# Performance work log

Measured on AMD Instinct MI355X. Metric: run time of the kernel, lower is better.

Reference implementation:

```python
import jax, jax.numpy as jnp
import numpy as np

B = 16384          # batch
N_IN = 1024        # input nodes
L = 8              # layers
W_LAYER = 512      # nodes per layer (fan-in and fan-out)
N_NODES = N_IN + L * W_LAYER  # 5120 total nodes in shared buffer
MASK_DENSITY = 0.25


def setup_inputs() -> dict:
    key = jax.random.key(0)
    kx, kw, km, kb = jax.random.split(key, 4)
    x = jax.random.normal(kx, (B, N_IN), dtype=jnp.float32)
    W = jax.random.normal(kw, (L, W_LAYER, W_LAYER), dtype=jnp.float32) * 0.05
    mask = (jax.random.uniform(km, (L, W_LAYER, W_LAYER)) < MASK_DENSITY).astype(jnp.float32)
    bias = jax.random.normal(kb, (L, W_LAYER), dtype=jnp.float32) * 0.01
    rng = np.random.default_rng(0)
    # layer l gathers from nodes already computed: indices in [0, N_IN + l*W_LAYER)
    in_idx = np.stack([rng.integers(0, N_IN + l * W_LAYER, size=W_LAYER) for l in range(L)]).astype(np.int32)
    # layer l writes its own contiguous node slots
    out_idx = np.stack([np.arange(N_IN + l * W_LAYER, N_IN + (l + 1) * W_LAYER) for l in range(L)]).astype(np.int32)
    return {"x": x, "W": W, "mask": mask, "bias": bias,
            "in_idx": jnp.asarray(in_idx), "out_idx": jnp.asarray(out_idx)}


def reference(x, W, mask, bias, in_idx, out_idx):
    # shared node-value buffer, inputs written into first N_IN columns
    values = jnp.zeros((x.shape[0], N_NODES), dtype=x.dtype)
    values = values.at[:, :N_IN].set(x)

    def step(vals, layer):
        idx_in, idx_out, Wl, ml, bl = layer
        node_inputs = vals[:, idx_in]                       # [B, W_LAYER] gather
        h = jax.nn.relu(node_inputs @ (Wl * ml).T + bl)     # masked linear + ReLU
        return vals.at[:, idx_out].set(h), None             # scatter back

    values, _ = jax.lax.scan(step, values, (in_idx, out_idx, W, mask, bias))
    return values[:, out_idx[-1]]  # output nodes = last layer's nodes
```

## Files before the change

kernel.cpp:

```cpp
#include <hip/hip_runtime.h>
#include <stdint.h>

typedef unsigned short u16;
typedef unsigned int   u32;
typedef short s16x8 __attribute__((ext_vector_type(8)));
typedef float f32x4 __attribute__((ext_vector_type(4)));

#define NB    16384
#define NIN   1024
#define WLY   512
#define NLAY  8
#define NNODE (NIN + NLAY * WLY)
#define BN    64

__device__ __forceinline__ u16 f2bf(float f) {
  union { float f; u32 u; } c; c.f = f;
  return (u16)((c.u + 0x7fffu + ((c.u >> 16) & 1u)) >> 16);
}

__global__ void prep_w(const float* __restrict__ W, const float* __restrict__ Mk,
                       u16* __restrict__ Wm) {
  int id   = blockIdx.x * 256 + threadIdx.x;
  int lane = id & 63;
  int chunk = id >> 6;
  int kf = chunk & 1;
  int mb = (chunk >> 1) & 31;
  int kt = (chunk >> 6) & 7;
  int l  = chunk >> 9;
  int m  = (mb << 4) + (lane & 15);
  int k0 = (kt << 6) + (kf << 5) + ((lane >> 4) << 3);
  size_t base = ((size_t)l << 18) + (size_t)m * 512 + k0;
  const float4* w4 = (const float4*)(W + base);
  const float4* k4 = (const float4*)(Mk + base);
  float4 w0 = w4[0], w1 = w4[1];
  float4 k0v = k4[0], k1v = k4[1];
  u32 p0 = (u32)f2bf(w0.x * k0v.x) | ((u32)f2bf(w0.y * k0v.y) << 16);
  u32 p1 = (u32)f2bf(w0.z * k0v.z) | ((u32)f2bf(w0.w * k0v.w) << 16);
  u32 p2 = (u32)f2bf(w1.x * k1v.x) | ((u32)f2bf(w1.y * k1v.y) << 16);
  u32 p3 = (u32)f2bf(w1.z * k1v.z) | ((u32)f2bf(w1.w * k1v.w) << 16);
  uint4 v; v.x = p0; v.y = p1; v.z = p2; v.w = p3;
  *(uint4*)(Wm + ((size_t)chunk << 9) + (lane << 3)) = v;
}

__global__ __launch_bounds__(512, 2) void fused_net(
    const float* __restrict__ x, const u16* __restrict__ Wfrag,
    const float* __restrict__ bias, const int* __restrict__ in_idx,
    u16* __restrict__ V, float* __restrict__ out) {

  __shared__ __align__(16) u16 Graw[2][4096];
  __shared__ __align__(16) u16 Gswz[2][4096];
  __shared__ int   idx_s[512];
  __shared__ float bias_s[512];
  __shared__ __align__(16) u16 Ebuf[512 * 72];

  int t = threadIdx.x;
  int lane = t & 63, w = t >> 6;
  int mlane = lane & 15, g = lane >> 4;
  int n0 = blockIdx.x * BN;

  float* xt = (float*)Ebuf;
  for (int cc = 0; cc < 8; ++cc) {
    #pragma unroll
    for (int it = 0; it < 4; ++it) {
      int cl = t + it * 512;
      int b = cl >> 5, p = cl & 31;
      *(float4*)(xt + b * 128 + (p << 2)) =
          *(const float4*)(x + (size_t)(n0 + b) * 1024 + cc * 128 + (p << 2));
    }
    __syncthreads();
    {
      int c = t >> 2, seg = t & 3;
      u32 p[8];
      #pragma unroll
      for (int i = 0; i < 8; ++i) {
        u16 lo = f2bf(xt[(seg * 16 + 2 * i) * 128 + c]);
        u16 hi = f2bf(xt[(seg * 16 + 2 * i + 1) * 128 + c]);
        p[i] = (u32)lo | ((u32)hi << 16);
      }
      u16* dst = V + (size_t)(cc * 128 + c) * NB + n0 + seg * 16;
      uint4 v0; v0.x = p[0]; v0.y = p[1]; v0.z = p[2]; v0.w = p[3];
      uint4 v1; v1.x = p[4]; v1.y = p[5]; v1.z = p[6]; v1.w = p[7];
      *(uint4*)dst = v0;
      *(uint4*)(dst + 8) = v1;
    }
    __syncthreads();
  }

#define STAGE(KT, BUF) do {                                                    \
    int k_ = (w << 3) + (lane >> 3);                                           \
    int row_ = idx_s[((KT) << 6) + k_];                                        \
    const u16* src_ = V + (size_t)row_ * NB + n0 + ((lane & 7) << 3);          \
    __builtin_amdgcn_global_load_lds(                                          \
        (const __attribute__((address_space(1))) u32*)src_,                    \
        (__attribute__((address_space(3))) u32*)(&Graw[BUF][w << 9]), 16, 0, 0); \
  } while (0)

  for (int l = 0; l < NLAY; ++l) {
    idx_s[t]  = in_idx[(l << 9) + t];
    bias_s[t] = bias[(l << 9) + t];
    __syncthreads();

    const u16* Wl = Wfrag + ((size_t)l << 18);
    int node_out = NIN + l * WLY;

    f32x4 acc[4][4];
    #pragma unroll
    for (int i = 0; i < 4; ++i)
      #pragma unroll
      for (int j = 0; j < 4; ++j)
        acc[i][j] = (f32x4){0.f, 0.f, 0.f, 0.f};

    STAGE(0, 0);
    __syncthreads();

    #pragma unroll
    for (int kt = 0; kt < 8; ++kt) {
      const int cur = kt & 1;
      s16x8 a[4][2];
      #pragma unroll
      for (int mb = 0; mb < 4; ++mb)
        #pragma unroll
        for (int kf = 0; kf < 2; ++kf)
          a[mb][kf] = *(const s16x8*)(Wl +
              ((size_t)(((kt * 32 + (w << 2) + mb) << 1) + kf) << 9) + (lane << 3));
      {
        int n = t & 63, kc = t >> 6;
        u32 p[4];
        #pragma unroll
        for (int i = 0; i < 4; ++i) {
          u16 lo = Graw[cur][(kc * 8 + 2 * i) * 64 + n];
          u16 hi = Graw[cur][(kc * 8 + 2 * i + 1) * 64 + n];
          p[i] = (u32)lo | ((u32)hi << 16);
        }
        uint4 vv; vv.x = p[0]; vv.y = p[1]; vv.z = p[2]; vv.w = p[3];
        *(uint4*)((char*)Gswz[cur] + n * 128 + ((kc * 16) ^ ((n & 7) << 4))) = vv;
      }
      if (kt < 7) { STAGE(kt + 1, cur ^ 1); }
      __syncthreads();
      #pragma unroll
      for (int kf = 0; kf < 2; ++kf) {
        s16x8 bfr[4];
        #pragma unroll
        for (int nf = 0; nf < 4; ++nf) {
          int n = (nf << 4) + mlane;
          bfr[nf] = *(const s16x8*)((const char*)Gswz[cur] + n * 128 +
                                    (((kf << 6) + (g << 4)) ^ ((n & 7) << 4)));
        }
        #pragma unroll
        for (int mb = 0; mb < 4; ++mb)
          #pragma unroll
          for (int nf = 0; nf < 4; ++nf)
            acc[mb][nf] = __builtin_amdgcn_mfma_f32_16x16x32_bf16(
                a[mb][kf], bfr[nf], acc[mb][nf], 0, 0, 0);
      }
    }

    if (l < NLAY - 1) {
      #pragma unroll
      for (int mb = 0; mb < 4; ++mb)
        #pragma unroll
        for (int nf = 0; nf < 4; ++nf)
          #pragma unroll
          for (int r = 0; r < 4; ++r) {
            int m = (w << 6) + (mb << 4) + (g << 2) + r;
            int n = (nf << 4) + mlane;
            Ebuf[m * 72 + n] = f2bf(fmaxf(acc[mb][nf][r] + bias_s[m], 0.f));
          }
      __syncthreads();
      #pragma unroll
      for (int it = 0; it < 8; ++it) {
        int row = (it << 6) + (t >> 3), part = t & 7;
        *(uint4*)(V + (size_t)(node_out + row) * NB + n0 + (part << 3)) =
            *(uint4*)(&Ebuf[row * 72 + (part << 3)]);
      }
      __syncthreads();
    } else {
      #pragma unroll
      for (int mb = 0; mb < 4; ++mb)
        #pragma unroll
        for (int nf = 0; nf < 4; ++nf) {
          int n = (nf << 4) + mlane;
          int m0f = (w << 6) + (mb << 4) + (g << 2);
          float4 v;
          v.x = fmaxf(acc[mb][nf][0] + bias_s[m0f + 0], 0.f);
          v.y = fmaxf(acc[mb][nf][1] + bias_s[m0f + 1], 0.f);
          v.z = fmaxf(acc[mb][nf][2] + bias_s[m0f + 2], 0.f);
          v.w = fmaxf(acc[mb][nf][3] + bias_s[m0f + 3], 0.f);
          *(float4*)(out + (size_t)(n0 + n) * 512 + m0f) = v;
        }
    }
  }
#undef STAGE
}

extern "C" void kernel_launch(void* const* d_in, const int* in_sizes, int n_in,
                              void* d_out, int out_size, void* d_ws, size_t ws_size,
                              hipStream_t stream) {
  (void)in_sizes; (void)n_in; (void)out_size; (void)ws_size;
  const float* x    = (const float*)d_in[0];
  const float* W    = (const float*)d_in[1];
  const float* Mk   = (const float*)d_in[2];
  const float* bias = (const float*)d_in[3];
  const int*  inidx = (const int*)d_in[4];
  float* out = (float*)d_out;

  char* ws = (char*)d_ws;
  u16* V     = (u16*)ws;
  u16* Wfrag = (u16*)(ws + (size_t)NNODE * NB * 2);

  prep_w<<<dim3(1024), 256, 0, stream>>>(W, Mk, Wfrag);
  fused_net<<<dim3(256), 512, 0, stream>>>(x, Wfrag, bias, inidx, V, out);
}
```

Measured before the change: 124.7 us.

## Deepen gather pipeline to four stages with manual waitcnt scheduling

Replaces the double-buffered gather/GEMM loop with a 4-deep Graw ring buffer, prefetching three k-tiles ahead and double-buffering the weight fragment registers. Explicit vmcnt/lgkmcnt waits and sched barriers replace the __syncthreads calls so global gathers overlap with the transpose and the MFMA work. The epilogue drops its barriers by having each wave write back only its own rows. The last layer is now staged through LDS in bf16 so stores to the output are coalesced. The tradeoffs are more LDS and registers, possible occupancy loss, bf16 rounding of the final output, and fragile hand-counted waits.

```diff
diff --git a/kernel.cpp b/kernel.cpp
--- a/kernel.cpp
+++ b/kernel.cpp
@@ -17,6 +17,16 @@
   union { float f; u32 u; } c; c.f = f;
   return (u16)((c.u + 0x7fffu + ((c.u >> 16) & 1u)) >> 16);
 }
+__device__ __forceinline__ float bf2f(u16 h) {
+  union { u32 u; float f; } c; c.u = ((u32)h) << 16;
+  return c.f;
+}
+
+#define SCHED0() __builtin_amdgcn_sched_barrier(0)
+#define BAR()    __builtin_amdgcn_s_barrier()
+#define WAITVM_IMPL(N) asm volatile("s_waitcnt vmcnt(" #N ")" ::: "memory")
+#define WAITVM(N) WAITVM_IMPL(N)
+#define WAITLG()  asm volatile("s_waitcnt lgkmcnt(0)" ::: "memory")
 
 __global__ void prep_w(const float* __restrict__ W, const float* __restrict__ Mk,
                        u16* __restrict__ Wm) {
@@ -47,11 +57,11 @@
     const float* __restrict__ bias, const int* __restrict__ in_idx,
     u16* __restrict__ V, float* __restrict__ out) {
 
-  __shared__ __align__(16) u16 Graw[2][4096];
+  __shared__ __align__(16) u16 Graw[4][4096];
   __shared__ __align__(16) u16 Gswz[2][4096];
+  __shared__ __align__(16) u16 Ebuf[512 * 72];
   __shared__ int   idx_s[512];
   __shared__ float bias_s[512];
-  __shared__ __align__(16) u16 Ebuf[512 * 72];
 
   int t = threadIdx.x;
   int lane = t & 63, w = t >> 6;
@@ -86,13 +96,63 @@
     __syncthreads();
   }
 
-#define STAGE(KT, BUF) do {                                                    \
+#define STAGE(KT, R) do {                                                      \
     int k_ = (w << 3) + (lane >> 3);                                           \
     int row_ = idx_s[((KT) << 6) + k_];                                        \
     const u16* src_ = V + (size_t)row_ * NB + n0 + ((lane & 7) << 3);          \
     __builtin_amdgcn_global_load_lds(                                          \
         (const __attribute__((address_space(1))) u32*)src_,                    \
-        (__attribute__((address_space(3))) u32*)(&Graw[BUF][w << 9]), 16, 0, 0); \
+        (__attribute__((address_space(3))) u32*)(&Graw[R][w << 9]), 16, 0, 0); \
+  } while (0)
+
+#define LDA(KTN) do {                                                          \
+    _Pragma("unroll") for (int mb = 0; mb < 4; ++mb)                           \
+    _Pragma("unroll") for (int kf = 0; kf < 2; ++kf)                           \
+      a[(KTN) & 1][mb][kf] = *(const s16x8*)(Wl +                              \
+          ((size_t)((((KTN) * 32 + (w << 2) + mb) << 1) + kf) << 9) +          \
+          (lane << 3));                                                        \
+  } while (0)
+
+#define TRANSP(KT) do {                                                        \
+    int n_ = t & 63, kc_ = t >> 6;                                             \
+    const u16* gb_ = Graw[(KT) & 3];                                           \
+    u32 p0_ = (u32)gb_[(kc_ * 8 + 0) * 64 + n_] |                              \
+              ((u32)gb_[(kc_ * 8 + 1) * 64 + n_] << 16);                       \
+    u32 p1_ = (u32)gb_[(kc_ * 8 + 2) * 64 + n_] |                              \
+              ((u32)gb_[(kc_ * 8 + 3) * 64 + n_] << 16);                       \
+    u32 p2_ = (u32)gb_[(kc_ * 8 + 4) * 64 + n_] |                              \
+              ((u32)gb_[(kc_ * 8 + 5) * 64 + n_] << 16);                       \
+    u32 p3_ = (u32)gb_[(kc_ * 8 + 6) * 64 + n_] |                              \
+              ((u32)gb_[(kc_ * 8 + 7) * 64 + n_] << 16);                       \
+    uint4 vv_; vv_.x = p0_; vv_.y = p1_; vv_.z = p2_; vv_.w = p3_;             \
+    *(uint4*)((char*)Gswz[(KT) & 1] + n_ * 128 +                               \
+              ((kc_ * 16) ^ ((n_ & 7) << 4))) = vv_;                           \
+  } while (0)
+
+#define MM(KT) do {                                                            \
+    const char* gs_ = (const char*)Gswz[(KT) & 1];                             \
+    _Pragma("unroll") for (int kf = 0; kf < 2; ++kf) {                         \
+      s16x8 bfr[4];                                                            \
+      _Pragma("unroll") for (int nf = 0; nf < 4; ++nf) {                       \
+        int n_ = (nf << 4) + mlane;                                            \
+        bfr[nf] = *(const s16x8*)(gs_ + n_ * 128 +                             \
+                  (((kf << 6) + (g << 4)) ^ ((n_ & 7) << 4)));                 \
+      }                                                                        \
+      _Pragma("unroll") for (int mb = 0; mb < 4; ++mb)                         \
+      _Pragma("unroll") for (int nf = 0; nf < 4; ++nf)                         \
+        acc[mb][nf] = __builtin_amdgcn_mfma_f32_16x16x32_bf16(                 \
+            a[(KT) & 1][mb][kf], bfr[nf], acc[mb][nf], 0, 0, 0);               \
+    }                                                                          \
+  } while (0)
+
+#define BODY(KT, VMN, PRE, POST) do {                                          \
+    if (PRE) { LDA((KT) + 1); }                                                \
+    SCHED0(); WAITVM(VMN); SCHED0();                                           \
+    BAR();                                                                     \
+    if (POST) { STAGE((KT) + 3, ((KT) + 3) & 3); }                             \
+    TRANSP(KT);                                                                \
+    SCHED0(); WAITLG(); BAR(); SCHED0();                                       \
+    MM(KT);                                                                    \
   } while (0)
 
   for (int l = 0; l < NLAY; ++l) {
@@ -110,50 +170,21 @@
       for (int j = 0; j < 4; ++j)
         acc[i][j] = (f32x4){0.f, 0.f, 0.f, 0.f};
 
-    STAGE(0, 0);
-    __syncthreads();
-
-    #pragma unroll
-    for (int kt = 0; kt < 8; ++kt) {
-      const int cur = kt & 1;
-      s16x8 a[4][2];
-      #pragma unroll
-      for (int mb = 0; mb < 4; ++mb)
-        #pragma unroll
-        for (int kf = 0; kf < 2; ++kf)
-          a[mb][kf] = *(const s16x8*)(Wl +
-              ((size_t)(((kt * 32 + (w << 2) + mb) << 1) + kf) << 9) + (lane << 3));
-      {
-        int n = t & 63, kc = t >> 6;
-        u32 p[4];
-        #pragma unroll
-        for (int i = 0; i < 4; ++i) {
-          u16 lo = Graw[cur][(kc * 8 + 2 * i) * 64 + n];
-          u16 hi = Graw[cur][(kc * 8 + 2 * i + 1) * 64 + n];
-          p[i] = (u32)lo | ((u32)hi << 16);
-        }
-        uint4 vv; vv.x = p[0]; vv.y = p[1]; vv.z = p[2]; vv.w = p[3];
-        *(uint4*)((char*)Gswz[cur] + n * 128 + ((kc * 16) ^ ((n & 7) << 4))) = vv;
-      }
-      if (kt < 7) { STAGE(kt + 1, cur ^ 1); }
-      __syncthreads();
-      #pragma unroll
-      for (int kf = 0; kf < 2; ++kf) {
-        s16x8 bfr[4];
-        #pragma unroll
-        for (int nf = 0; nf < 4; ++nf) {
-          int n = (nf << 4) + mlane;
-          bfr[nf] = *(const s16x8*)((const char*)Gswz[cur] + n * 128 +
-                                    (((kf << 6) + (g << 4)) ^ ((n & 7) << 4)));
-        }
-        #pragma unroll
-        for (int mb = 0; mb < 4; ++mb)
-          #pragma unroll
-          for (int nf = 0; nf < 4; ++nf)
-            acc[mb][nf] = __builtin_amdgcn_mfma_f32_16x16x32_bf16(
-                a[mb][kf], bfr[nf], acc[mb][nf], 0, 0, 0);
-      }
-    }
+    s16x8 a[2][4][2];
+
+    STAGE(0, 0); STAGE(1, 1); STAGE(2, 2);
+    SCHED0();
+    LDA(0);
+    SCHED0();
+
+    BODY(0, 8, 1, 1);
+    BODY(1, 9, 1, 1);
+    BODY(2, 9, 1, 1);
+    BODY(3, 9, 1, 1);
+    BODY(4, 9, 1, 1);
+    BODY(5, 9, 1, 0);
+    BODY(6, 8, 1, 0);
+    BODY(7, 0, 0, 0);
 
     if (l < NLAY - 1) {
       #pragma unroll
@@ -166,31 +197,44 @@
             int n = (nf << 4) + mlane;
             Ebuf[m * 72 + n] = f2bf(fmaxf(acc[mb][nf][r] + bias_s[m], 0.f));
           }
-      __syncthreads();
       #pragma unroll
       for (int it = 0; it < 8; ++it) {
-        int row = (it << 6) + (t >> 3), part = t & 7;
-        *(uint4*)(V + (size_t)(node_out + row) * NB + n0 + (part << 3)) =
-            *(uint4*)(&Ebuf[row * 72 + (part << 3)]);
+        int row = (w << 6) + (it << 3) + (lane >> 3);
+        uint4 vv = *(uint4*)(Ebuf + row * 72 + ((lane & 7) << 3));
+        *(uint4*)(V + (size_t)(node_out + row) * NB + n0 + ((lane & 7) << 3)) = vv;
       }
-      __syncthreads();
     } else {
       #pragma unroll
       for (int mb = 0; mb < 4; ++mb)
         #pragma unroll
-        for (int nf = 0; nf < 4; ++nf) {
-          int n = (nf << 4) + mlane;
-          int m0f = (w << 6) + (mb << 4) + (g << 2);
+        for (int nf = 0; nf < 4; ++nf)
+          #pragma unroll
+          for (int r = 0; r < 4; ++r) {
+            int m = (w << 6) + (mb << 4) + (g << 2) + r;
+            int n = (nf << 4) + mlane;
+            Ebuf[m * 66 + n] = f2bf(fmaxf(acc[mb][nf][r] + bias_s[m], 0.f));
+          }
+      __syncthreads();
+      #pragma unroll
+      for (int pn = 0; pn < 8; ++pn)
+        #pragma unroll
+        for (int h = 0; h < 2; ++h) {
+          int n = (t >> 6) + (pn << 3);
+          int mbase = ((t & 63) << 2) + (h << 8);
           float4 v;
-          v.x = fmaxf(acc[mb][nf][0] + bias_s[m0f + 0], 0.f);
-          v.y = fmaxf(acc[mb][nf][1] + bias_s[m0f + 1], 0.f);
-          v.z = fmaxf(acc[mb][nf][2] + bias_s[m0f + 2], 0.f);
-          v.w = fmaxf(acc[mb][nf][3] + bias_s[m0f + 3], 0.f);
-          *(float4*)(out + (size_t)(n0 + n) * 512 + m0f) = v;
+          v.x = bf2f(Ebuf[(mbase + 0) * 66 + n]);
+          v.y = bf2f(Ebuf[(mbase + 1) * 66 + n]);
+          v.z = bf2f(Ebuf[(mbase + 2) * 66 + n]);
+          v.w = bf2f(Ebuf[(mbase + 3) * 66 + n]);
+          *(float4*)(out + (size_t)(n0 + n) * 512 + mbase) = v;
         }
     }
   }
 #undef STAGE
+#undef LDA
+#undef TRANSP
+#undef MM
+#undef BODY
 }
 
 extern "C" void kernel_launch(void* const* d_in, const int* in_sizes, int n_in,
```

After: 123.2 us. No clear change (-1.2%).

## Halve batch tile to 32, shrink LDS pool, raise occupancy

Applied to the files above, without the earlier changes.

Batch tile per block drops from 64 to 32 columns, doubling the grid to 512 blocks and asking for 4 blocks per CU. LDS shrinks to a single 16 KB pool. The epilogue LDS staging buffer is removed, so activations go straight to global memory as strided 2-byte stores. Bias and index arrays are read from global into registers rather than shared memory. The aim is more resident waves and lower LDS and barrier cost, but each block now does fewer MFMAs per weight fragment loaded, doubling total weight traffic, and the direct scattered 2-byte writes are poorly coalesced.

```diff
diff --git a/kernel.cpp b/kernel.cpp
--- a/kernel.cpp
+++ b/kernel.cpp
@@ -11,7 +11,7 @@
 #define WLY   512
 #define NLAY  8
 #define NNODE (NIN + NLAY * WLY)
-#define BN    64
+#define BN    32
 
 __device__ __forceinline__ u16 f2bf(float f) {
   union { float f; u32 u; } c; c.f = f;
@@ -42,26 +42,24 @@
   *(uint4*)(Wm + ((size_t)chunk << 9) + (lane << 3)) = v;
 }
 
-__global__ __launch_bounds__(512, 2) void fused_net(
+__global__ __launch_bounds__(512, 4) void fused_net(
     const float* __restrict__ x, const u16* __restrict__ Wfrag,
     const float* __restrict__ bias, const int* __restrict__ in_idx,
     u16* __restrict__ V, float* __restrict__ out) {
 
-  __shared__ __align__(16) u16 Graw[2][4096];
-  __shared__ __align__(16) u16 Gswz[2][4096];
-  __shared__ int   idx_s[512];
-  __shared__ float bias_s[512];
-  __shared__ __align__(16) u16 Ebuf[512 * 72];
+  __shared__ __align__(16) u16 pool[8192];
+  u16* Graw0 = pool;
+  u16* Gswz0 = pool + 4096;
 
   int t = threadIdx.x;
   int lane = t & 63, w = t >> 6;
   int mlane = lane & 15, g = lane >> 4;
   int n0 = blockIdx.x * BN;
 
-  float* xt = (float*)Ebuf;
+  float* xt = (float*)pool;
   for (int cc = 0; cc < 8; ++cc) {
     #pragma unroll
-    for (int it = 0; it < 4; ++it) {
+    for (int it = 0; it < 2; ++it) {
       int cl = t + it * 512;
       int b = cl >> 5, p = cl & 31;
       *(float4*)(xt + b * 128 + (p << 2)) =
@@ -70,127 +68,132 @@
     __syncthreads();
     {
       int c = t >> 2, seg = t & 3;
-      u32 p[8];
-      #pragma unroll
-      for (int i = 0; i < 8; ++i) {
-        u16 lo = f2bf(xt[(seg * 16 + 2 * i) * 128 + c]);
-        u16 hi = f2bf(xt[(seg * 16 + 2 * i + 1) * 128 + c]);
-        p[i] = (u32)lo | ((u32)hi << 16);
-      }
-      u16* dst = V + (size_t)(cc * 128 + c) * NB + n0 + seg * 16;
-      uint4 v0; v0.x = p[0]; v0.y = p[1]; v0.z = p[2]; v0.w = p[3];
-      uint4 v1; v1.x = p[4]; v1.y = p[5]; v1.z = p[6]; v1.w = p[7];
-      *(uint4*)dst = v0;
-      *(uint4*)(dst + 8) = v1;
+      u32 pk[4];
+      #pragma unroll
+      for (int i = 0; i < 4; ++i) {
+        u16 lo = f2bf(xt[(seg * 8 + 2 * i) * 128 + c]);
+        u16 hi = f2bf(xt[(seg * 8 + 2 * i + 1) * 128 + c]);
+        pk[i] = (u32)lo | ((u32)hi << 16);
+      }
+      uint4 vv; vv.x = pk[0]; vv.y = pk[1]; vv.z = pk[2]; vv.w = pk[3];
+      *(uint4*)(V + (size_t)(cc * 128 + c) * NB + n0 + (seg << 3)) = vv;
     }
     __syncthreads();
   }
 
-#define STAGE(KT, BUF) do {                                                    \
-    int k_ = (w << 3) + (lane >> 3);                                           \
-    int row_ = idx_s[((KT) << 6) + k_];                                        \
-    const u16* src_ = V + (size_t)row_ * NB + n0 + ((lane & 7) << 3);          \
-    __builtin_amdgcn_global_load_lds(                                          \
-        (const __attribute__((address_space(1))) u32*)src_,                    \
-        (__attribute__((address_space(3))) u32*)(&Graw[BUF][w << 9]), 16, 0, 0); \
-  } while (0)
-
   for (int l = 0; l < NLAY; ++l) {
-    idx_s[t]  = in_idx[(l << 9) + t];
-    bias_s[t] = bias[(l << 9) + t];
-    __syncthreads();
-
+    __syncthreads();
+
+    int rowv[8];
+    if (w < 4) {
+      #pragma unroll
+      for (int kt = 0; kt < 8; ++kt)
+        rowv[kt] = in_idx[(l << 9) + (kt << 6) + (w << 4) + (lane >> 2)];
+    }
     const u16* Wl = Wfrag + ((size_t)l << 18);
     int node_out = NIN + l * WLY;
 
-    f32x4 acc[4][4];
+    f32x4 acc[4][2];
     #pragma unroll
     for (int i = 0; i < 4; ++i)
       #pragma unroll
-      for (int j = 0; j < 4; ++j)
+      for (int j = 0; j < 2; ++j)
         acc[i][j] = (f32x4){0.f, 0.f, 0.f, 0.f};
+
+    s16x8 a[4][2];
+
+#define STAGE(KT, BUF) do {                                                    \
+    if (w < 4) {                                                               \
+      const u16* src_ = V + (size_t)rowv[KT] * NB + n0 + ((lane & 3) << 3);    \
+      __builtin_amdgcn_global_load_lds(                                        \
+          (const __attribute__((address_space(1))) u32*)src_,                  \
+          (__attribute__((address_space(3))) u32*)(Graw0 + ((BUF) << 11) +     \
+                                                  (w << 9)), 16, 0, 0);        \
+    }                                                                          \
+  } while (0)
 
     STAGE(0, 0);
     __syncthreads();
 
     #pragma unroll
     for (int kt = 0; kt < 8; ++kt) {
-      const int cur = kt & 1;
-      s16x8 a[4][2];
       #pragma unroll
       for (int mb = 0; mb < 4; ++mb)
         #pragma unroll
         for (int kf = 0; kf < 2; ++kf)
           a[mb][kf] = *(const s16x8*)(Wl +
-              ((size_t)(((kt * 32 + (w << 2) + mb) << 1) + kf) << 9) + (lane << 3));
+              ((size_t)(((kt * 32 + (w << 2) + mb) << 1) + kf) << 9) +
+              (lane << 3));
+      if (kt < 7) STAGE(kt + 1, (kt + 1) & 1);
       {
-        int n = t & 63, kc = t >> 6;
-        u32 p[4];
-        #pragma unroll
-        for (int i = 0; i < 4; ++i) {
-          u16 lo = Graw[cur][(kc * 8 + 2 * i) * 64 + n];
-          u16 hi = Graw[cur][(kc * 8 + 2 * i + 1) * 64 + n];
-          p[i] = (u32)lo | ((u32)hi << 16);
+        const u16* gb = Graw0 + ((kt & 1) << 11);
+        int n_ = t & 31, kc4 = t >> 5;
+        u16 v0 = gb[(kc4 * 4 + 0) * 32 + n_];
+        u16 v1 = gb[(kc4 * 4 + 1) * 32 + n_];
+        u16 v2 = gb[(kc4 * 4 + 2) * 32 + n_];
+        u16 v3 = gb[(kc4 * 4 + 3) * 32 + n_];
+        u32 p0 = (u32)v0 | ((u32)v1 << 16);
+        u32 p1 = (u32)v2 | ((u32)v3 << 16);
+        uint2 pr; pr.x = p0; pr.y = p1;
+        *(uint2*)((char*)(Gswz0 + ((kt & 1) << 11)) + n_ * 128 +
+                  ((kc4 << 3) ^ ((n_ & 7) << 4))) = pr;
+      }
+      __syncthreads();
+      {
+        const char* gs = (const char*)(Gswz0 + ((kt & 1) << 11));
+        #pragma unroll
+        for (int kf = 0; kf < 2; ++kf) {
+          s16x8 bfr[2];
+          #pragma unroll
+          for (int nf = 0; nf < 2; ++nf) {
+            int n_ = (nf << 4) + mlane;
+            bfr[nf] = *(const s16x8*)(gs + n_ * 128 +
+                      (((kf << 6) + (g << 4)) ^ ((n_ & 7) << 4)));
+          }
+          #pragma unroll
+          for (int mb = 0; mb < 4; ++mb)
+            #pragma unroll
+            for (int nf = 0; nf < 2; ++nf)
+              acc[mb][nf] = __builtin_amdgcn_mfma_f32_16x16x32_bf16(
+                  a[mb][kf], bfr[nf], acc[mb][nf], 0, 0, 0);
         }
-        uint4 vv; vv.x = p[0]; vv.y = p[1]; vv.z = p[2]; vv.w = p[3];
-        *(uint4*)((char*)Gswz[cur] + n * 128 + ((kc * 16) ^ ((n & 7) << 4))) = vv;
-      }
-      if (kt < 7) { STAGE(kt + 1, cur ^ 1); }
-      __syncthreads();
-      #pragma unroll
-      for (int kf = 0; kf < 2; ++kf) {
-        s16x8 bfr[4];
-        #pragma unroll
-        for (int nf = 0; nf < 4; ++nf) {
-          int n = (nf << 4) + mlane;
-          bfr[nf] = *(const s16x8*)((const char*)Gswz[cur] + n * 128 +
-                                    (((kf << 6) + (g << 4)) ^ ((n & 7) << 4)));
+      }
+    }
+#undef STAGE
+
+    if (l < NLAY - 1) {
+      #pragma unroll
+      for (int mb = 0; mb < 4; ++mb) {
+        float4 bv = *(const float4*)(bias + (l << 9) + (w << 6) + (mb << 4) + (g << 2));
+        float bvr[4] = {bv.x, bv.y, bv.z, bv.w};
+        #pragma unroll
+        for (int nf = 0; nf < 2; ++nf) {
+          int n_ = (nf << 4) + mlane;
+          u16* vp = V + (size_t)(node_out + (w << 6) + (mb << 4) + (g << 2)) * NB
+                      + n0 + n_;
+          #pragma unroll
+          for (int r = 0; r < 4; ++r)
+            vp[(size_t)r * NB] = f2bf(fmaxf(acc[mb][nf][r] + bvr[r], 0.f));
         }
-        #pragma unroll
-        for (int mb = 0; mb < 4; ++mb)
-          #pragma unroll
-          for (int nf = 0; nf < 4; ++nf)
-            acc[mb][nf] = __builtin_amdgcn_mfma_f32_16x16x32_bf16(
-                a[mb][kf], bfr[nf], acc[mb][nf], 0, 0, 0);
-      }
-    }
-
-    if (l < NLAY - 1) {
-      #pragma unroll
-      for (int mb = 0; mb < 4; ++mb)
-        #pragma unroll
-        for (int nf = 0; nf < 4; ++nf)
-          #pragma unroll
-          for (int r = 0; r < 4; ++r) {
-            int m = (w << 6) + (mb << 4) + (g << 2) + r;
-            int n = (nf << 4) + mlane;
-            Ebuf[m * 72 + n] = f2bf(fmaxf(acc[mb][nf][r] + bias_s[m], 0.f));
-          }
-      __syncthreads();
-      #pragma unroll
-      for (int it = 0; it < 8; ++it) {
-        int row = (it << 6) + (t >> 3), part = t & 7;
-        *(uint4*)(V + (size_t)(node_out + row) * NB + n0 + (part << 3)) =
-            *(uint4*)(&Ebuf[row * 72 + (part << 3)]);
-      }
-      __syncthreads();
+      }
     } else {
       #pragma unroll
-      for (int mb = 0; mb < 4; ++mb)
-        #pragma unroll
-        for (int nf = 0; nf < 4; ++nf) {
-          int n = (nf << 4) + mlane;
+      for (int mb = 0; mb < 4; ++mb) {
+        float4 bv = *(const float4*)(bias + (l << 9) + (w << 6) + (mb << 4) + (g << 2));
+        #pragma unroll
+        for (int nf = 0; nf < 2; ++nf) {
+          int n_ = (nf << 4) + mlane;
           int m0f = (w << 6) + (mb << 4) + (g << 2);
           float4 v;
-          v.x = fmaxf(acc[mb][nf][0] + bias_s[m0f + 0], 0.f);
-          v.y = fmaxf(acc[mb][nf][1] + bias_s[m0f + 1], 0.f);
-          v.z = fmaxf(acc[mb][nf][2] + bias_s[m0f + 2], 0.f);
-          v.w = fmaxf(acc[mb][nf][3] + bias_s[m0f + 3], 0.f);
-          *(float4*)(out + (size_t)(n0 + n) * 512 + m0f) = v;
+          v.x = fmaxf(acc[mb][nf][0] + bv.x, 0.f);
+          v.y = fmaxf(acc[mb][nf][1] + bv.y, 0.f);
+          v.z = fmaxf(acc[mb][nf][2] + bv.z, 0.f);
+          v.w = fmaxf(acc[mb][nf][3] + bv.w, 0.f);
+          *(float4*)(out + (size_t)(n0 + n_) * 512 + m0f) = v;
         }
+      }
     }
   }
-#undef STAGE
 }
 
 extern "C" void kernel_launch(void* const* d_in, const int* in_sizes, int n_in,
@@ -209,5 +212,5 @@
   u16* Wfrag = (u16*)(ws + (size_t)NNODE * NB * 2);
 
   prep_w<<<dim3(1024), 256, 0, stream>>>(W, Mk, Wfrag);
-  fused_net<<<dim3(256), 512, 0, stream>>>(x, Wfrag, bias, inidx, V, out);
-}
+  fused_net<<<dim3(512), 512, 0, stream>>>(x, Wfrag, bias, inidx, V, out);
+}
```

Measured after the change: 152.9 us. 22.7% more time.
